# Performance work log

Hardware: AMD Instinct MI355X
Metric: run time of the kernel (lower is better)

## Reference

```python
import jax, jax.numpy as jnp
import numpy as np

D = 1024; H = 16; HD = 64; L = 8; V = 2048; FF = 4096; WIN = 256
THETA = 10000.0; EPS = 1e-5; LN_EPS = 1e-5; MAXCYC = 16
NM = 16; NR = 72; NT = 12; ME = 64; RE = 64; TE = 32; TPE = 16; DE = 16
B = 2; S = 1024


def _rotate_half(x):
    # torch: stack((-x[...,1::2], x[...,0::2]), -1).flatten(-2)
    x1 = x[..., ::2]
    x2 = x[..., 1::2]
    return jnp.stack((-x2, x1), axis=-1).reshape(x.shape)


def _rmsnorm(x, w):
    return w * (x * jax.lax.rsqrt(jnp.mean(x * x, axis=-1, keepdims=True) + EPS))


def _layernorm(x, g, b):
    mu = jnp.mean(x, axis=-1, keepdims=True)
    var = jnp.mean((x - mu) ** 2, axis=-1, keepdims=True)
    return (x - mu) * jax.lax.rsqrt(var + LN_EPS) * g + b


def setup_inputs() -> dict:
    key = jax.random.key(0)
    ks = iter(jax.random.split(key, 64))
    w = lambda shape: jax.random.normal(next(ks), shape, jnp.float32) * 0.02
    inp = {
        'tokens': jax.random.randint(next(ks), (B, S), 0, V),
        'mood': jax.random.randint(next(ks), (B,), 0, NM),
        'raga': jax.random.randint(next(ks), (B,), 0, NR),
        'taal': jax.random.randint(next(ks), (B,), 0, NT),
        'tempo': jax.random.uniform(next(ks), (B,), jnp.float32),
        'duration': jax.random.uniform(next(ks), (B,), jnp.float32),
        'taal_cycle_len': 8,
        'tok_emb': w((V, D)),
        'mood_emb': w((NM, ME)), 'raga_emb': w((NR, RE)), 'taal_emb': w((NT, TE)),
        'tempo_w': w((TPE, 1)), 'tempo_b': jnp.zeros((TPE,), jnp.float32),
        'dur_w': w((DE, 1)), 'dur_b': jnp.zeros((DE,), jnp.float32),
        'proj_w': w((D, ME + RE + TE + TPE + DE)), 'proj_b': jnp.zeros((D,), jnp.float32),
        'ln_g': jnp.ones((D,), jnp.float32), 'ln_b': jnp.zeros((D,), jnp.float32),
        'cycle_emb': w((MAXCYC, D)), 'strength_emb': w((4, D)),
        'l_anorm': jnp.ones((L, D), jnp.float32), 'l_fnorm': jnp.ones((L, D), jnp.float32),
        'l_q': w((L, D, D)), 'l_k': w((L, D, D)), 'l_v': w((L, D, D)), 'l_o': w((L, D, D)),
        'l_w1': w((L, FF, D)), 'l_w2': w((L, D, FF)), 'l_w3': w((L, FF, D)),
        'final_norm': jnp.ones((D,), jnp.float32),
        'head_w': w((V, D)),
    }
    return inp


def reference(tokens, mood, raga, taal, tempo, duration, taal_cycle_len,
              tok_emb, mood_emb, raga_emb, taal_emb, tempo_w, tempo_b, dur_w, dur_b,
              proj_w, proj_b, ln_g, ln_b, cycle_emb, strength_emb,
              l_anorm, l_fnorm, l_q, l_k, l_v, l_o, l_w1, l_w2, l_w3,
              final_norm, head_w):
    bsz, seq_len = tokens.shape
    # --- ConditioningModule ---
    tp = tempo[:, None] * tempo_w[:, 0][None, :] + tempo_b      # Linear(1, TPE)
    dp = duration[:, None] * dur_w[:, 0][None, :] + dur_b       # Linear(1, DE)
    cond = jnp.concatenate([mood_emb[mood], raga_emb[raga], taal_emb[taal], tp, dp], axis=-1)
    cond = jax.nn.gelu(cond @ proj_w.T + proj_b, approximate=False)
    cond = _layernorm(cond, ln_g, ln_b)                          # [B, D]
    # --- TaalPositionEncoder (taal_cycle_len is static python int) ---
    cyc = min(int(taal_cycle_len), MAXCYC)
    pos_emb = cycle_emb[jnp.arange(seq_len) % cyc]
    strengths = jnp.full((seq_len,), 3, jnp.int32).at[::int(taal_cycle_len)].set(0)
    taal_pos = pos_emb + strength_emb[strengths]                 # [S, D]
    # --- input embedding ---
    x = tok_emb[tokens] + cond[:, None, :] + taal_pos[None]      # [B, S, D]
    # --- RoPE tables (scaling=1.0) ---
    inv_freq = 1.0 / (THETA ** (jnp.arange(0, HD, 2, jnp.float32) / HD))
    freqs = jnp.outer(jnp.arange(seq_len, dtype=jnp.float32), inv_freq)
    emb = jnp.concatenate([freqs, freqs], axis=-1)               # [S, HD]
    cos = jnp.cos(emb)[None, None]
    sin = jnp.sin(emb)[None, None]
    # --- causal sliding-window mask bias ---
    idx = jnp.arange(seq_len)
    allow = (idx[:, None] >= idx[None, :]) & (idx[:, None] - idx[None, :] < WIN)
    bias = jnp.where(allow, 0.0, -jnp.inf).astype(x.dtype)       # [S, S]
    scale = 1.0 / np.sqrt(HD)

    def block(x, p):
        an, fn, qw, kw, vw, ow, w1, w2, w3 = p
        h = _rmsnorm(x, an)
        q = (h @ qw.T).reshape(bsz, seq_len, H, HD).transpose(0, 2, 1, 3)
        k = (h @ kw.T).reshape(bsz, seq_len, H, HD).transpose(0, 2, 1, 3)
        v = (h @ vw.T).reshape(bsz, seq_len, H, HD).transpose(0, 2, 1, 3)
        q = q * cos + _rotate_half(q) * sin
        k = k * cos + _rotate_half(k) * sin
        scores = jnp.einsum('bhqd,bhkd->bhqk', q, k) * scale + bias
        attn = jax.nn.softmax(scores, axis=-1)
        y = jnp.einsum('bhqk,bhkd->bhqd', attn, v)
        y = y.transpose(0, 2, 1, 3).reshape(bsz, seq_len, D)
        x = x + y @ ow.T
        h2 = _rmsnorm(x, fn)
        x = x + (jax.nn.silu(h2 @ w1.T) * (h2 @ w3.T)) @ w2.T
        return x, None

    x, _ = jax.lax.scan(block, x, (l_anorm, l_fnorm, l_q, l_k, l_v, l_o, l_w1, l_w2, l_w3))
    x = _rmsnorm(x, final_norm)
    return x @ head_w.T                                          # [B, S, V] logits
```

## Files before the change

### kernel.cpp

```cpp
#include <hip/hip_runtime.h>
#include <math.h>

#define D_ 1024
#define H_ 16
#define HD_ 64
#define L_ 8
#define V_ 2048
#define FF_ 4096
#define WIN_ 256
#define B_ 2
#define S_ 1024
#define MAXCYC_ 16

typedef __attribute__((ext_vector_type(4))) float f32x4;
typedef __attribute__((ext_vector_type(8))) short s16x8;

__device__ __forceinline__ unsigned short f2bf(float f) {
  union { float f; unsigned int u; } v; v.f = f;
  unsigned int r = v.u + 0x7FFFu + ((v.u >> 16) & 1u);
  return (unsigned short)(r >> 16);
}

__device__ __forceinline__ float wave_sum(float v) {
  #pragma unroll
  for (int m = 1; m < 64; m <<= 1) v += __shfl_xor(v, m, 64);
  return v;
}

__device__ __forceinline__ void gload16(const unsigned short* g, unsigned short* lds) {
  __builtin_amdgcn_global_load_lds(
      (const __attribute__((address_space(1))) void*)g,
      (__attribute__((address_space(3))) void*)lds,
      16, 0, 0);
}

__global__ __launch_bounds__(256) void cvt_kernel(
    const float* __restrict__ src, unsigned short* __restrict__ dst, int n8)
{
  int i = blockIdx.x*256 + threadIdx.x;
  if (i >= n8) return;
  const float4* s = (const float4*)src + (size_t)i*2;
  float4 a = s[0], b = s[1];
  ushort4 lo, hi;
  lo.x = f2bf(a.x); lo.y = f2bf(a.y); lo.z = f2bf(a.z); lo.w = f2bf(a.w);
  hi.x = f2bf(b.x); hi.y = f2bf(b.y); hi.z = f2bf(b.z); hi.w = f2bf(b.w);
  *(ushort4*)(dst + (size_t)i*8)     = lo;
  *(ushort4*)(dst + (size_t)i*8 + 4) = hi;
}

__global__ __launch_bounds__(256) void cond_kernel(
    const int* mood, const int* raga, const int* taal,
    const float* tempo, const float* duration,
    const float* mood_emb, const float* raga_emb, const float* taal_emb,
    const float* tempo_w, const float* tempo_b, const float* dur_w, const float* dur_b,
    const float* proj_w, const float* proj_b, const float* ln_g, const float* ln_b,
    float* cond)
{
  int b = blockIdx.x;
  int t = threadIdx.x;
  __shared__ float feat[192];
  __shared__ float red[4];
  if (t < 64)        feat[t] = mood_emb[mood[b]*64 + t];
  else if (t < 128)  feat[t] = raga_emb[raga[b]*64 + (t-64)];
  else if (t < 160)  feat[t] = taal_emb[taal[b]*32 + (t-128)];
  else if (t < 176)  feat[t] = tempo[b]*tempo_w[t-160] + tempo_b[t-160];
  else if (t < 192)  feat[t] = duration[b]*dur_w[t-176] + dur_b[t-176];
  __syncthreads();
  float g[4];
  #pragma unroll
  for (int r = 0; r < 4; ++r) {
    int j = t + 256*r;
    const float* w = proj_w + (size_t)j*192;
    float acc = proj_b[j];
    for (int f = 0; f < 192; ++f) acc += feat[f]*w[f];
    g[r] = 0.5f * acc * (1.0f + erff(acc * 0.7071067811865475f));
  }
  int lane = t & 63, wv = t >> 6;
  float s1 = g[0]+g[1]+g[2]+g[3];
  s1 = wave_sum(s1);
  if (lane == 0) red[wv] = s1;
  __syncthreads();
  float mu = (red[0]+red[1]+red[2]+red[3]) * (1.0f/1024.0f);
  __syncthreads();
  float vs = 0.f;
  #pragma unroll
  for (int r = 0; r < 4; ++r) { float d = g[r]-mu; vs += d*d; }
  vs = wave_sum(vs);
  if (lane == 0) red[wv] = vs;
  __syncthreads();
  float var = (red[0]+red[1]+red[2]+red[3]) * (1.0f/1024.0f);
  float is = rsqrtf(var + 1e-5f);
  #pragma unroll
  for (int r = 0; r < 4; ++r) {
    int j = t + 256*r;
    cond[(size_t)b*D_ + j] = (g[r]-mu)*is*ln_g[j] + ln_b[j];
  }
}

__global__ __launch_bounds__(256) void embed_kernel(
    const int* tokens, const float* tok_emb, const float* cond,
    const float* cycle_emb, const float* strength_emb, const int* tcl_p, float* x)
{
  int row = blockIdx.x;
  int b = row >> 10, s = row & 1023;
  int tcl = tcl_p[0];
  int cyc = tcl < MAXCYC_ ? tcl : MAXCYC_;
  int pr  = s % cyc;
  int str = (s % tcl == 0) ? 0 : 3;
  int tok = tokens[row];
  int d = threadIdx.x * 4;
  float4 a = *(const float4*)&tok_emb[(size_t)tok*D_ + d];
  float4 c = *(const float4*)&cond[(size_t)b*D_ + d];
  float4 p = *(const float4*)&cycle_emb[(size_t)pr*D_ + d];
  float4 e = *(const float4*)&strength_emb[(size_t)str*D_ + d];
  float4 o; o.x=a.x+c.x+p.x+e.x; o.y=a.y+c.y+p.y+e.y; o.z=a.z+c.z+p.z+e.z; o.w=a.w+c.w+p.w+e.w;
  *(float4*)&x[(size_t)row*D_ + d] = o;
}

__global__ __launch_bounds__(256) void rmsnorm_kernel(
    const float* x, const float* w, unsigned short* out)
{
  int row = blockIdx.x;
  int t = threadIdx.x;
  __shared__ float red[4];
  const float* xr = x + (size_t)row*D_;
  float4 v = *(const float4*)&xr[t*4];
  float ss = v.x*v.x + v.y*v.y + v.z*v.z + v.w*v.w;
  ss = wave_sum(ss);
  int lane = t & 63, wv = t >> 6;
  if (lane == 0) red[wv] = ss;
  __syncthreads();
  float total = red[0]+red[1]+red[2]+red[3];
  float scale = rsqrtf(total * (1.0f/1024.0f) + 1e-5f);
  float4 wv4 = *(const float4*)&w[t*4];
  ushort4 o;
  o.x = f2bf(wv4.x * v.x * scale);
  o.y = f2bf(wv4.y * v.y * scale);
  o.z = f2bf(wv4.z * v.z * scale);
  o.w = f2bf(wv4.w * v.w * scale);
  *(ushort4*)&out[(size_t)row*D_ + t*4] = o;
}

__global__ __launch_bounds__(256) void resid_rmsnorm_kernel(
    float* __restrict__ x, const float* __restrict__ part, int nparts,
    const float* __restrict__ w, unsigned short* __restrict__ out)
{
  int row = blockIdx.x;
  int t = threadIdx.x;
  __shared__ float red[4];
  size_t base = (size_t)row*D_ + t*4;
  const size_t pstride = (size_t)B_*S_*D_;
  float4 v = *(const float4*)&x[base];
  for (int p = 0; p < nparts; ++p) {
    float4 a = *(const float4*)&part[p*pstride + base];
    v.x += a.x; v.y += a.y; v.z += a.z; v.w += a.w;
  }
  *(float4*)&x[base] = v;
  float ss = v.x*v.x + v.y*v.y + v.z*v.z + v.w*v.w;
  ss = wave_sum(ss);
  int lane = t & 63, wv = t >> 6;
  if (lane == 0) red[wv] = ss;
  __syncthreads();
  float total = red[0]+red[1]+red[2]+red[3];
  float scale = rsqrtf(total * (1.0f/1024.0f) + 1e-5f);
  float4 wv4 = *(const float4*)&w[t*4];
  ushort4 o;
  o.x = f2bf(wv4.x * v.x * scale);
  o.y = f2bf(wv4.y * v.y * scale);
  o.z = f2bf(wv4.z * v.z * scale);
  o.w = f2bf(wv4.w * v.w * scale);
  *(ushort4*)&out[(size_t)row*D_ + t*4] = o;
}

__global__ __launch_bounds__(256) void rope_table_kernel(float* costab, float* sintab)
{
  int i = blockIdx.x*256 + threadIdx.x;
  int s = i >> 6, d = i & 63;
  float inv = powf(10000.0f, -(float)(d & 31) * (1.0f/32.0f));
  float ang = (float)s * inv;
  float sn, cs;
  sincosf(ang, &sn, &cs);
  costab[i] = cs; sintab[i] = sn;
}

__global__ __launch_bounds__(256) void attn_mfma(
    const unsigned short* __restrict__ q, const unsigned short* __restrict__ k,
    const unsigned short* __restrict__ v, unsigned short* __restrict__ y)
{
  __shared__ unsigned short Ks[64*64];
  __shared__ unsigned short VsT[64*72];
  __shared__ unsigned short Ps[4*16*72];

  int qb0 = blockIdx.x * 64;
  int h = blockIdx.y, b = blockIdx.z;
  int t = threadIdx.x, lane = t & 63, wv = t >> 6;
  int c = lane & 15, q4 = lane >> 4;
  unsigned short* Pw = &Ps[wv*16*72];

  s16x8 aq[2];
  {
    const unsigned short* qp =
        q + ((size_t)(b*S_ + qb0 + wv*16 + c)*D_ + h*HD_ + q4*8);
    aq[0] = *(const s16x8*)qp;
    aq[1] = *(const s16x8*)(qp + 32);
  }

  f32x4 o[4];
  #pragma unroll
  for (int j = 0; j < 4; ++j) o[j] = (f32x4){0.f,0.f,0.f,0.f};
  float m[4] = {-1e30f,-1e30f,-1e30f,-1e30f};
  float l[4] = {0.f,0.f,0.f,0.f};

  int skey = t >> 2;
  int scol = (t & 3) * 16;
  int kt0 = qb0 - 256; if (kt0 < 0) kt0 = 0;

  for (int kt = kt0; kt <= qb0; kt += 64) {
    __syncthreads();
    {
      const unsigned short* kp = k + ((size_t)(b*S_ + kt + skey)*D_ + h*HD_ + scol);
      s16x8 k0 = *(const s16x8*)kp;
      s16x8 k1 = *(const s16x8*)(kp + 8);
      int ch0 = scol >> 3;
      *(s16x8*)((char*)Ks + skey*128 + ((ch0 ^ (skey & 7)) << 4)) = k0;
      *(s16x8*)((char*)Ks + skey*128 + (((ch0+1) ^ (skey & 7)) << 4)) = k1;
      const unsigned short* vp = v + ((size_t)(b*S_ + kt + skey)*D_ + h*HD_ + scol);
      s16x8 v0 = *(const s16x8*)vp;
      s16x8 v1 = *(const s16x8*)(vp + 8);
      #pragma unroll
      for (int i = 0; i < 8; ++i) {
        VsT[(scol + i)*72 + skey]     = (unsigned short)v0[i];
        VsT[(scol + 8 + i)*72 + skey] = (unsigned short)v1[i];
      }
    }
    __syncthreads();

    f32x4 sa[4];
    #pragma unroll
    for (int j = 0; j < 4; ++j) sa[j] = (f32x4){0.f,0.f,0.f,0.f};
    #pragma unroll
    for (int ks = 0; ks < 2; ++ks)
      #pragma unroll
      for (int j = 0; j < 4; ++j) {
        int key = j*16 + c;
        s16x8 bk = *(const s16x8*)((const char*)Ks + key*128 +
                                   (((q4 + ks*4) ^ (key & 7)) << 4));
        sa[j] = __builtin_amdgcn_mfma_f32_16x16x32_bf16(aq[ks], bk, sa[j], 0, 0, 0);
      }

    float sv[4][4];
    #pragma unroll
    for (int j = 0; j < 4; ++j) {
      int kg = kt + j*16 + c;
      #pragma unroll
      for (int reg = 0; reg < 4; ++reg) {
        int qg = qb0 + wv*16 + q4*4 + reg;
        bool ok = (qg >= kg) && (qg - kg < WIN_);
        sv[j][reg] = ok ? sa[j][reg]*0.125f : -3e38f;
      }
    }
    #pragma unroll
    for (int reg = 0; reg < 4; ++reg) {
      float mx = fmaxf(fmaxf(sv[0][reg], sv[1][reg]), fmaxf(sv[2][reg], sv[3][reg]));
      #pragma unroll
      for (int msk = 1; msk < 16; msk <<= 1)
        mx = fmaxf(mx, __shfl_xor(mx, msk, 64));
      float nm = fmaxf(m[reg], mx);
      float f = __expf(m[reg] - nm);
      m[reg] = nm;
      l[reg] *= f;
      o[0][reg] *= f; o[1][reg] *= f; o[2][reg] *= f; o[3][reg] *= f;
      float ps = 0.f;
      #pragma unroll
      for (int j = 0; j < 4; ++j) {
        float p = __expf(sv[j][reg] - nm);
        ps += p;
        Pw[(q4*4 + reg)*72 + j*16 + c] = f2bf(p);
      }
      l[reg] += ps;
    }

    #pragma unroll
    for (int ks = 0; ks < 2; ++ks) {
      s16x8 pa = *(const s16x8*)((const char*)Pw + c*144 + (q4 + ks*4)*16);
      #pragma unroll
      for (int j = 0; j < 4; ++j) {
        s16x8 bv = *(const s16x8*)((const char*)VsT + (j*16 + c)*144 + (q4 + ks*4)*16);
        o[j] = __builtin_amdgcn_mfma_f32_16x16x32_bf16(pa, bv, o[j], 0, 0, 0);
      }
    }
  }

  float inv[4];
  #pragma unroll
  for (int reg = 0; reg < 4; ++reg) {
    float ll = l[reg];
    #pragma unroll
    for (int msk = 1; msk < 16; msk <<= 1) ll += __shfl_xor(ll, msk, 64);
    inv[reg] = 1.0f / ll;
  }
  #pragma unroll
  for (int j = 0; j < 4; ++j)
    #pragma unroll
    for (int reg = 0; reg < 4; ++reg)
      Pw[(q4*4 + reg)*72 + j*16 + c] = f2bf(o[j][reg] * inv[reg]);
  int lr = lane >> 2, cc = (lane & 3)*16;
  s16x8 y0 = *(const s16x8*)((const char*)Pw + lr*144 + cc*2);
  s16x8 y1 = *(const s16x8*)((const char*)Pw + lr*144 + cc*2 + 16);
  unsigned short* yp = y + ((size_t)(b*S_ + qb0 + wv*16 + lr)*D_ + h*HD_ + cc);
  *(s16x8*)yp = y0;
  *(s16x8*)(yp + 8) = y1;
}

__global__ __launch_bounds__(256, 2) void gemm_w13(
    const unsigned short* __restrict__ A,
    const unsigned short* __restrict__ W1, const unsigned short* __restrict__ W3,
    unsigned short* __restrict__ T, int K, int lda, int ldw)
{
  __shared__ unsigned short sA[2][128*32];
  __shared__ unsigned short sW1[2][128*32];
  __shared__ unsigned short sW3[2][128*32];
  int tid = threadIdx.x, lane = tid & 63, wave = tid >> 6;
  int wr = (wave >> 1)*64, wc = (wave & 1)*64;
  size_t bm = (size_t)blockIdx.x*128, bn = (size_t)blockIdx.y*128;
  int fr = lane & 15, q4 = lane >> 4, fq = q4*4;
  int lrow = lane >> 2;
  int gcol = ((lane & 3) ^ (lrow & 3)) * 8;

  f32x4 a1[4][4], a3[4][4];
  #pragma unroll
  for (int i = 0; i < 4; ++i)
    #pragma unroll
    for (int j = 0; j < 4; ++j) {
      a1[i][j] = (f32x4){0.f,0.f,0.f,0.f};
      a3[i][j] = (f32x4){0.f,0.f,0.f,0.f};
    }

  auto stage = [&](int buf, int kt) {
    #pragma unroll
    for (int p = 0; p < 2; ++p) {
      int seg = wave*2 + p;
      size_t row = (size_t)(seg*16 + lrow);
      gload16(A  + (bm + row)*(size_t)lda + kt + gcol, &sA[buf][seg*512]);
      gload16(W1 + (bn + row)*(size_t)ldw + kt + gcol, &sW1[buf][seg*512]);
      gload16(W3 + (bn + row)*(size_t)ldw + kt + gcol, &sW3[buf][seg*512]);
    }
  };

  stage(0, 0);
  __syncthreads();
  int nt = K >> 5;
  for (int t = 0; t < nt; ++t) {
    int cur = t & 1;
    if (t + 1 < nt) stage(cur ^ 1, (t+1)*32);
    s16x8 af[4], b1[4], b3[4];
    #pragma unroll
    for (int i = 0; i < 4; ++i) {
      int ra = wr + i*16 + fr, rb = wc + i*16 + fr;
      af[i] = *(const s16x8*)((const char*)&sA[cur][0]  + ra*64 + ((q4 ^ (ra & 3)) << 4));
      b1[i] = *(const s16x8*)((const char*)&sW1[cur][0] + rb*64 + ((q4 ^ (rb & 3)) << 4));
      b3[i] = *(const s16x8*)((const char*)&sW3[cur][0] + rb*64 + ((q4 ^ (rb & 3)) << 4));
    }
    #pragma unroll
    for (int i = 0; i < 4; ++i)
      #pragma unroll
      for (int j = 0; j < 4; ++j) {
        a1[i][j] = __builtin_amdgcn_mfma_f32_16x16x32_bf16(af[i], b1[j], a1[i][j], 0, 0, 0);
        a3[i][j] = __builtin_amdgcn_mfma_f32_16x16x32_bf16(af[i], b3[j], a3[i][j], 0, 0, 0);
      }
    __syncthreads();
  }

  #pragma unroll
  for (int i = 0; i < 4; ++i)
    #pragma unroll
    for (int j = 0; j < 4; ++j) {
      size_t row0 = bm + wr + i*16 + fq;
      size_t col  = bn + wc + j*16 + fr;
      #pragma unroll
      for (int qi = 0; qi < 4; ++qi) {
        float u = a1[i][j][qi];
        float g = a3[i][j][qi];
        float su = u / (1.0f + __expf(-u));
        T[(row0 + qi)*(size_t)FF_ + col] = f2bf(su * g);
      }
    }
}

template<int EPI>
__device__ __forceinline__ void gemm64_core(
    const unsigned short* __restrict__ A, const unsigned short* __restrict__ W,
    float* __restrict__ Cf, unsigned short* __restrict__ Cb,
    int kbase, int Kslice, int lda, int ldw, int ldc,
    const float* __restrict__ costab, const float* __restrict__ sintab)
{
  __shared__ unsigned short sA[2][128*64];
  __shared__ unsigned short sW[2][64*64];
  int tid = threadIdx.x, lane = tid & 63, wave = tid >> 6;
  int wr = (wave >> 1)*64, wc = (wave & 1)*32;
  size_t bm = (size_t)blockIdx.x*128, bn = (size_t)blockIdx.y*64;
  int fr = lane & 15, q4 = lane >> 4, fq = q4*4;
  int lrow = lane >> 3;
  int gcol = ((lane & 7) ^ lrow) * 8;

  f32x4 acc[4][2];
  #pragma unroll
  for (int i = 0; i < 4; ++i) {
    acc[i][0] = (f32x4){0.f,0.f,0.f,0.f};
    acc[i][1] = (f32x4){0.f,0.f,0.f,0.f};
  }

  auto stage = [&](int buf, int kt) {
    #pragma unroll
    for (int p = 0; p < 4; ++p) {
      int seg = wave*4 + p;
      gload16(A + (bm + seg*8 + lrow)*(size_t)lda + kt + gcol, &sA[buf][seg*512]);
    }
    #pragma unroll
    for (int p = 0; p < 2; ++p) {
      int seg = wave*2 + p;
      gload16(W + (bn + seg*8 + lrow)*(size_t)ldw + kt + gcol, &sW[buf][seg*512]);
    }
  };

  stage(0, kbase);
  __syncthreads();
  int nt = Kslice >> 6;
  for (int t = 0; t < nt; ++t) {
    int cur = t & 1;
    if (t + 1 < nt) stage(cur ^ 1, kbase + (t+1)*64);
    #pragma unroll
    for (int ks = 0; ks < 2; ++ks) {
      s16x8 af[4], bw[2];
      #pragma unroll
      for (int i = 0; i < 4; ++i) {
        int r = wr + i*16 + fr;
        af[i] = *(const s16x8*)((const char*)&sA[cur][0] + r*128 +
                                ((((ks<<2) + q4) ^ (r & 7)) << 4));
      }
      #pragma unroll
      for (int j = 0; j < 2; ++j) {
        int r = wc + j*16 + fr;
        bw[j] = *(const s16x8*)((const char*)&sW[cur][0] + r*128 +
                                ((((ks<<2) + q4) ^ (r & 7)) << 4));
      }
      #pragma unroll
      for (int i = 0; i < 4; ++i)
        #pragma unroll
        for (int j = 0; j < 2; ++j)
          acc[i][j] = __builtin_amdgcn_mfma_f32_16x16x32_bf16(af[i], bw[j], acc[i][j], 0, 0, 0);
    }
    __syncthreads();
  }

  #pragma unroll
  for (int i = 0; i < 4; ++i)
    #pragma unroll
    for (int j = 0; j < 2; ++j) {
      size_t row0 = bm + wr + i*16 + fq;
      size_t col  = bn + wc + j*16 + fr;
      #pragma unroll
      for (int qi = 0; qi < 4; ++qi) {
        float val = acc[i][j][qi];
        size_t idx = (row0 + qi)*(size_t)ldc + col;
        if (EPI == 3) {
          float pv = __shfl_xor(val, 1, 64);
          int srow = (int)((row0 + qi) & 1023);
          int d = (int)(col & 63);
          float cs = costab[srow*64 + d];
          float sn = sintab[srow*64 + d];
          Cb[idx] = f2bf(val*cs + ((d & 1) ? pv : -pv)*sn);
        } else if (EPI == 4) {
          Cb[idx] = f2bf(val);
        } else {
          Cf[idx] = val;
        }
      }
    }
}

template<int EPI>
__global__ __launch_bounds__(256, 3) void gemm64(
    const unsigned short* __restrict__ A, const unsigned short* __restrict__ W,
    float* __restrict__ Cf, int K, int lda, int ldw, int ldc)
{
  gemm64_core<EPI>(A, W, Cf, nullptr, 0, K, lda, ldw, ldc, nullptr, nullptr);
}

__global__ __launch_bounds__(256, 3) void gemm64_ksplit(
    const unsigned short* __restrict__ A, const unsigned short* __restrict__ W,
    float* __restrict__ P, int Kslice, int lda, int ldw, int ldc)
{
  float* out = P + (size_t)blockIdx.z * (size_t)B_ * S_ * ldc;
  gemm64_core<0>(A, W, out, nullptr, blockIdx.z*Kslice, Kslice, lda, ldw, ldc,
                 nullptr, nullptr);
}

__global__ __launch_bounds__(256, 3) void gemm_qkv64(
    const unsigned short* __restrict__ A,
    const unsigned short* __restrict__ Wq, const unsigned short* __restrict__ Wk,
    const unsigned short* __restrict__ Wv,
    unsigned short* __restrict__ Cq, unsigned short* __restrict__ Ck,
    unsigned short* __restrict__ Cv,
    const float* __restrict__ costab, const float* __restrict__ sintab)
{
  if (blockIdx.z == 0)
    gemm64_core<3>(A, Wq, nullptr, Cq, 0, D_, D_, D_, D_, costab, sintab);
  else if (blockIdx.z == 1)
    gemm64_core<3>(A, Wk, nullptr, Ck, 0, D_, D_, D_, D_, costab, sintab);
  else
    gemm64_core<4>(A, Wv, nullptr, Cv, 0, D_, D_, D_, D_, nullptr, nullptr);
}

extern "C" void kernel_launch(void* const* d_in, const int* in_sizes, int n_in,
                              void* d_out, int out_size, void* d_ws, size_t ws_size,
                              hipStream_t stream)
{
  const int*   tokens    = (const int*)d_in[0];
  const int*   mood      = (const int*)d_in[1];
  const int*   raga      = (const int*)d_in[2];
  const int*   taal      = (const int*)d_in[3];
  const float* tempo     = (const float*)d_in[4];
  const float* duration  = (const float*)d_in[5];
  const int*   tcl       = (const int*)d_in[6];
  const float* tok_emb   = (const float*)d_in[7];
  const float* mood_emb  = (const float*)d_in[8];
  const float* raga_emb  = (const float*)d_in[9];
  const float* taal_emb  = (const float*)d_in[10];
  const float* tempo_w   = (const float*)d_in[11];
  const float* tempo_b   = (const float*)d_in[12];
  const float* dur_w     = (const float*)d_in[13];
  const float* dur_b     = (const float*)d_in[14];
  const float* proj_w    = (const float*)d_in[15];
  const float* proj_b    = (const float*)d_in[16];
  const float* ln_g      = (const float*)d_in[17];
  const float* ln_b      = (const float*)d_in[18];
  const float* cycle_emb = (const float*)d_in[19];
  const float* strength_e= (const float*)d_in[20];
  const float* l_anorm   = (const float*)d_in[21];
  const float* l_fnorm   = (const float*)d_in[22];
  const float* l_q       = (const float*)d_in[23];
  const float* l_k       = (const float*)d_in[24];
  const float* l_v       = (const float*)d_in[25];
  const float* l_o       = (const float*)d_in[26];
  const float* l_w1      = (const float*)d_in[27];
  const float* l_w2      = (const float*)d_in[28];
  const float* l_w3      = (const float*)d_in[29];
  const float* final_norm= (const float*)d_in[30];
  const float* head_w    = (const float*)d_in[31];

  size_t off = 0;
  char* wsb = (char*)d_ws;
  auto alloc = [&](size_t bytes) -> char* {
    char* p = wsb + off;
    off += (bytes + 255) & ~(size_t)255;
    return p;
  };
  float*          condb  = (float*)alloc((size_t)B_*D_*4);
  float*          costab = (float*)alloc((size_t)S_*HD_*4);
  float*          sintab = (float*)alloc((size_t)S_*HD_*4);
  float*          x      = (float*)alloc((size_t)B_*S_*D_*4);
  unsigned short* hbuf   = (unsigned short*)alloc((size_t)B_*S_*D_*2);
  unsigned short* qb     = (unsigned short*)alloc((size_t)B_*S_*D_*2);
  unsigned short* kb     = (unsigned short*)alloc((size_t)B_*S_*D_*2);
  unsigned short* vb     = (unsigned short*)alloc((size_t)B_*S_*D_*2);
  unsigned short* yb     = (unsigned short*)alloc((size_t)B_*S_*D_*2);
  unsigned short* tb     = (unsigned short*)alloc((size_t)B_*S_*FF_*2);
  float*          pbuf   = (float*)alloc((size_t)4*B_*S_*D_*4);

  const size_t N_QKVO = (size_t)L_*D_*D_;
  const size_t N_FF   = (size_t)L_*FF_*D_;
  const size_t N_HEAD = (size_t)V_*D_;
  unsigned short* wbf = (unsigned short*)alloc((4*N_QKVO + 3*N_FF + N_HEAD)*2);
  unsigned short* bq = wbf;
  unsigned short* bk = wbf + N_QKVO;
  unsigned short* bv = wbf + 2*N_QKVO;
  unsigned short* bo = wbf + 3*N_QKVO;
  unsigned short* b1 = wbf + 4*N_QKVO;
  unsigned short* b2 = wbf + 4*N_QKVO + N_FF;
  unsigned short* b3 = wbf + 4*N_QKVO + 2*N_FF;
  unsigned short* bh = wbf + 4*N_QKVO + 3*N_FF;

  rope_table_kernel<<<(S_*HD_)/256, 256, 0, stream>>>(costab, sintab);
  cond_kernel<<<B_, 256, 0, stream>>>(mood, raga, taal, tempo, duration,
      mood_emb, raga_emb, taal_emb, tempo_w, tempo_b, dur_w, dur_b,
      proj_w, proj_b, ln_g, ln_b, condb);
  embed_kernel<<<B_*S_, 256, 0, stream>>>(tokens, tok_emb, condb, cycle_emb,
      strength_e, tcl, x);

  cvt_kernel<<<(int)(N_QKVO/8/256), 256, 0, stream>>>(l_q,  bq, (int)(N_QKVO/8));
  cvt_kernel<<<(int)(N_QKVO/8/256), 256, 0, stream>>>(l_k,  bk, (int)(N_QKVO/8));
  cvt_kernel<<<(int)(N_QKVO/8/256), 256, 0, stream>>>(l_v,  bv, (int)(N_QKVO/8));
  cvt_kernel<<<(int)(N_QKVO/8/256), 256, 0, stream>>>(l_o,  bo, (int)(N_QKVO/8));
  cvt_kernel<<<(int)(N_FF/8/256),   256, 0, stream>>>(l_w1, b1, (int)(N_FF/8));
  cvt_kernel<<<(int)(N_FF/8/256),   256, 0, stream>>>(l_w2, b2, (int)(N_FF/8));
  cvt_kernel<<<(int)(N_FF/8/256),   256, 0, stream>>>(l_w3, b3, (int)(N_FF/8));
  cvt_kernel<<<(int)(N_HEAD/8/256), 256, 0, stream>>>(head_w, bh, (int)(N_HEAD/8));

  const int rows = B_*S_;
  rmsnorm_kernel<<<rows, 256, 0, stream>>>(x, l_anorm, hbuf);
  for (int l = 0; l < L_; ++l) {
    size_t dd = (size_t)l*D_*D_;
    size_t fd = (size_t)l*FF_*D_;
    gemm_qkv64<<<dim3(rows/128, D_/64, 3), 256, 0, stream>>>(
        hbuf, bq + dd, bk + dd, bv + dd, qb, kb, vb, costab, sintab);
    attn_mfma<<<dim3(S_/64, H_, B_), 256, 0, stream>>>(qb, kb, vb, yb);
    gemm64_ksplit<<<dim3(rows/128, D_/64, 2), 256, 0, stream>>>(
        yb, bo + dd, pbuf, 512, D_, D_, D_);
    resid_rmsnorm_kernel<<<rows, 256, 0, stream>>>(
        x, pbuf, 2, l_fnorm + (size_t)l*D_, hbuf);
    gemm_w13<<<dim3(rows/128, FF_/128), 256, 0, stream>>>(
        hbuf, b1 + fd, b3 + fd, tb, D_, D_, D_);
    gemm64_ksplit<<<dim3(rows/128, D_/64, 4), 256, 0, stream>>>(
        tb, b2 + fd, pbuf, 1024, FF_, FF_, D_);
    const float* nextw = (l+1 < L_) ? (l_anorm + (size_t)(l+1)*D_) : final_norm;
    resid_rmsnorm_kernel<<<rows, 256, 0, stream>>>(x, pbuf, 4, nextw, hbuf);
  }
  gemm64<0><<<dim3(rows/128, V_/64), 256, 0, stream>>>(
      hbuf, bh, (float*)d_out, D_, D_, D_, V_);
}
```

Measured before the change: 1.782 ms.

## Triple-buffer GEMM LDS staging with explicit vmcnt waits and MFMA priority

Both GEMM kernels move from double-buffered to triple-buffered LDS staging with prefetch distance two. The __syncthreads calls are replaced by explicit s_waitcnt vmcnt counts plus raw s_barrier, so global loads for tile t+2 stay in flight while tile t is computed. The 64-wide GEMM core drops its K tile from 64 to 32 and both kernels switch to a new XOR swizzle keyed on row>>1. MFMA sections in the GEMMs and in attention are wrapped in s_setprio to favour matrix issue. The risks are that the hand-counted vmcnt values must exactly match the number of gload16 calls per stage, and that the smaller K tile doubles the number of barrier iterations.

```diff
diff --git a/kernel.cpp b/kernel.cpp
--- a/kernel.cpp
+++ b/kernel.cpp
@@ -238,6 +238,7 @@
     f32x4 sa[4];
     #pragma unroll
     for (int j = 0; j < 4; ++j) sa[j] = (f32x4){0.f,0.f,0.f,0.f};
+    __builtin_amdgcn_s_setprio(1);
     #pragma unroll
     for (int ks = 0; ks < 2; ++ks)
       #pragma unroll
@@ -247,6 +248,7 @@
                                    (((q4 + ks*4) ^ (key & 7)) << 4));
         sa[j] = __builtin_amdgcn_mfma_f32_16x16x32_bf16(aq[ks], bk, sa[j], 0, 0, 0);
       }
+    __builtin_amdgcn_s_setprio(0);
 
     float sv[4][4];
     #pragma unroll
@@ -280,6 +282,7 @@
       l[reg] += ps;
     }
 
+    __builtin_amdgcn_s_setprio(1);
     #pragma unroll
     for (int ks = 0; ks < 2; ++ks) {
       s16x8 pa = *(const s16x8*)((const char*)Pw + c*144 + (q4 + ks*4)*16);
@@ -289,6 +292,7 @@
         o[j] = __builtin_amdgcn_mfma_f32_16x16x32_bf16(pa, bv, o[j], 0, 0, 0);
       }
     }
+    __builtin_amdgcn_s_setprio(0);
   }
 
   float inv[4];
@@ -317,15 +321,15 @@
     const unsigned short* __restrict__ W1, const unsigned short* __restrict__ W3,
     unsigned short* __restrict__ T, int K, int lda, int ldw)
 {
-  __shared__ unsigned short sA[2][128*32];
-  __shared__ unsigned short sW1[2][128*32];
-  __shared__ unsigned short sW3[2][128*32];
+  __shared__ unsigned short sA[3][128*32];
+  __shared__ unsigned short sW1[3][128*32];
+  __shared__ unsigned short sW3[3][128*32];
   int tid = threadIdx.x, lane = tid & 63, wave = tid >> 6;
   int wr = (wave >> 1)*64, wc = (wave & 1)*64;
   size_t bm = (size_t)blockIdx.x*128, bn = (size_t)blockIdx.y*128;
   int fr = lane & 15, q4 = lane >> 4, fq = q4*4;
   int lrow = lane >> 2;
-  int gcol = ((lane & 3) ^ (lrow & 3)) * 8;
+  int gcol = ((lane & 3) ^ ((lrow >> 1) & 3)) * 8;
 
   f32x4 a1[4][4], a3[4][4];
   #pragma unroll
@@ -347,20 +351,31 @@
     }
   };
 
+  int nt = K >> 5;
   stage(0, 0);
-  __syncthreads();
-  int nt = K >> 5;
+  stage(1, 32);
   for (int t = 0; t < nt; ++t) {
-    int cur = t & 1;
-    if (t + 1 < nt) stage(cur ^ 1, (t+1)*32);
+    int cur = t % 3;
+    if (t + 2 < nt) {
+      stage((t+2)%3, (t+2)*32);
+      asm volatile("s_waitcnt vmcnt(12)" ::: "memory");
+    } else if (t + 1 < nt) {
+      asm volatile("s_waitcnt vmcnt(6)" ::: "memory");
+    } else {
+      asm volatile("s_waitcnt vmcnt(0)" ::: "memory");
+    }
+    __builtin_amdgcn_sched_barrier(0);
+    __builtin_amdgcn_s_barrier();
+    __builtin_amdgcn_sched_barrier(0);
     s16x8 af[4], b1[4], b3[4];
     #pragma unroll
     for (int i = 0; i < 4; ++i) {
       int ra = wr + i*16 + fr, rb = wc + i*16 + fr;
-      af[i] = *(const s16x8*)((const char*)&sA[cur][0]  + ra*64 + ((q4 ^ (ra & 3)) << 4));
-      b1[i] = *(const s16x8*)((const char*)&sW1[cur][0] + rb*64 + ((q4 ^ (rb & 3)) << 4));
-      b3[i] = *(const s16x8*)((const char*)&sW3[cur][0] + rb*64 + ((q4 ^ (rb & 3)) << 4));
-    }
+      af[i] = *(const s16x8*)((const char*)&sA[cur][0]  + ra*64 + ((q4 ^ ((ra>>1)&3)) << 4));
+      b1[i] = *(const s16x8*)((const char*)&sW1[cur][0] + rb*64 + ((q4 ^ ((rb>>1)&3)) << 4));
+      b3[i] = *(const s16x8*)((const char*)&sW3[cur][0] + rb*64 + ((q4 ^ ((rb>>1)&3)) << 4));
+    }
+    __builtin_amdgcn_s_setprio(1);
     #pragma unroll
     for (int i = 0; i < 4; ++i)
       #pragma unroll
@@ -368,7 +383,10 @@
         a1[i][j] = __builtin_amdgcn_mfma_f32_16x16x32_bf16(af[i], b1[j], a1[i][j], 0, 0, 0);
         a3[i][j] = __builtin_amdgcn_mfma_f32_16x16x32_bf16(af[i], b3[j], a3[i][j], 0, 0, 0);
       }
-    __syncthreads();
+    __builtin_amdgcn_s_setprio(0);
+    __builtin_amdgcn_sched_barrier(0);
+    __builtin_amdgcn_s_barrier();
+    __builtin_amdgcn_sched_barrier(0);
   }
 
   #pragma unroll
@@ -394,14 +412,14 @@
     int kbase, int Kslice, int lda, int ldw, int ldc,
     const float* __restrict__ costab, const float* __restrict__ sintab)
 {
-  __shared__ unsigned short sA[2][128*64];
-  __shared__ unsigned short sW[2][64*64];
+  __shared__ unsigned short sA[3][128*32];
+  __shared__ unsigned short sW[3][64*32];
   int tid = threadIdx.x, lane = tid & 63, wave = tid >> 6;
   int wr = (wave >> 1)*64, wc = (wave & 1)*32;
   size_t bm = (size_t)blockIdx.x*128, bn = (size_t)blockIdx.y*64;
   int fr = lane & 15, q4 = lane >> 4, fq = q4*4;
-  int lrow = lane >> 3;
-  int gcol = ((lane & 7) ^ lrow) * 8;
+  int lrow = lane >> 2;
+  int gcol = ((lane & 3) ^ ((lrow >> 1) & 3)) * 8;
 
   f32x4 acc[4][2];
   #pragma unroll
@@ -412,45 +430,50 @@
 
   auto stage = [&](int buf, int kt) {
     #pragma unroll
-    for (int p = 0; p < 4; ++p) {
-      int seg = wave*4 + p;
-      gload16(A + (bm + seg*8 + lrow)*(size_t)lda + kt + gcol, &sA[buf][seg*512]);
-    }
-    #pragma unroll
     for (int p = 0; p < 2; ++p) {
       int seg = wave*2 + p;
-      gload16(W + (bn + seg*8 + lrow)*(size_t)ldw + kt + gcol, &sW[buf][seg*512]);
-    }
+      gload16(A + (bm + seg*16 + lrow)*(size_t)lda + kt + gcol, &sA[buf][seg*512]);
+    }
+    gload16(W + (bn + wave*16 + lrow)*(size_t)ldw + kt + gcol, &sW[buf][wave*512]);
   };
 
+  int nt = Kslice >> 5;
   stage(0, kbase);
-  __syncthreads();
-  int nt = Kslice >> 6;
+  stage(1, kbase + 32);
   for (int t = 0; t < nt; ++t) {
-    int cur = t & 1;
-    if (t + 1 < nt) stage(cur ^ 1, kbase + (t+1)*64);
-    #pragma unroll
-    for (int ks = 0; ks < 2; ++ks) {
-      s16x8 af[4], bw[2];
-      #pragma unroll
-      for (int i = 0; i < 4; ++i) {
-        int r = wr + i*16 + fr;
-        af[i] = *(const s16x8*)((const char*)&sA[cur][0] + r*128 +
-                                ((((ks<<2) + q4) ^ (r & 7)) << 4));
-      }
-      #pragma unroll
-      for (int j = 0; j < 2; ++j) {
-        int r = wc + j*16 + fr;
-        bw[j] = *(const s16x8*)((const char*)&sW[cur][0] + r*128 +
-                                ((((ks<<2) + q4) ^ (r & 7)) << 4));
-      }
-      #pragma unroll
-      for (int i = 0; i < 4; ++i)
-        #pragma unroll
-        for (int j = 0; j < 2; ++j)
-          acc[i][j] = __builtin_amdgcn_mfma_f32_16x16x32_bf16(af[i], bw[j], acc[i][j], 0, 0, 0);
-    }
-    __syncthreads();
+    int cur = t % 3;
+    if (t + 2 < nt) {
+      stage((t+2)%3, kbase + (t+2)*32);
+      asm volatile("s_waitcnt vmcnt(6)" ::: "memory");
+    } else if (t + 1 < nt) {
+      asm volatile("s_waitcnt vmcnt(3)" ::: "memory");
+    } else {
+      asm volatile("s_waitcnt vmcnt(0)" ::: "memory");
+    }
+    __builtin_amdgcn_sched_barrier(0);
+    __builtin_amdgcn_s_barrier();
+    __builtin_amdgcn_sched_barrier(0);
+    s16x8 af[4], bw[2];
+    #pragma unroll
+    for (int i = 0; i < 4; ++i) {
+      int r = wr + i*16 + fr;
+      af[i] = *(const s16x8*)((const char*)&sA[cur][0] + r*64 + ((q4 ^ ((r>>1)&3)) << 4));
+    }
+    #pragma unroll
+    for (int j = 0; j < 2; ++j) {
+      int r = wc + j*16 + fr;
+      bw[j] = *(const s16x8*)((const char*)&sW[cur][0] + r*64 + ((q4 ^ ((r>>1)&3)) << 4));
+    }
+    __builtin_amdgcn_s_setprio(1);
+    #pragma unroll
+    for (int i = 0; i < 4; ++i)
+      #pragma unroll
+      for (int j = 0; j < 2; ++j)
+        acc[i][j] = __builtin_amdgcn_mfma_f32_16x16x32_bf16(af[i], bw[j], acc[i][j], 0, 0, 0);
+    __builtin_amdgcn_s_setprio(0);
+    __builtin_amdgcn_sched_barrier(0);
+    __builtin_amdgcn_s_barrier();
+    __builtin_amdgcn_sched_barrier(0);
   }
 
   #pragma unroll
```

Measured after the change: 1.583 ms. 11.1% less time.
